# Kernel optimization log

Measured on AMD Instinct MI355X. Metric: run time of the kernel, lower is better.

Reference implementation:

```python
import jax, jax.numpy as jnp
import numpy as np


def setup_inputs() -> dict:
    key = jax.random.key(0)
    k1, k2, k3 = jax.random.split(key, 3)
    B, S, D_IN, V, D_OUT = 2, 2048, 1024, 32000, 4096
    x = jax.random.normal(k1, (B, S, D_IN), dtype=jnp.float32)
    W_ff = jax.random.normal(k2, (V, D_IN), dtype=jnp.float32) * (1.0 / np.sqrt(D_IN))
    b_ff = jnp.zeros((V,), dtype=jnp.float32)
    emb = jax.random.normal(k3, (V, D_OUT), dtype=jnp.float32)
    return {"x": x, "W_ff": W_ff, "b_ff": b_ff, "emb": emb}


def reference(x, W_ff, b_ff, emb):
    # logits: [B, S, V] = x @ W_ff^T + b
    logits = jnp.einsum('bsd,vd->bsv', x, W_ff) + b_ff
    probs = jax.nn.softmax(logits, axis=-1)  # [B, S, V]
    # soft embedding lookup: probs @ emb -> [B, S, D_OUT]
    out = jnp.einsum('bsv,vo->bso', probs, emb)
    return out
```

## Files before the change

### kernel.cpp

```cpp
#include <hip/hip_runtime.h>
#include <cstdint>

typedef unsigned short u16;
typedef __attribute__((ext_vector_type(8))) short short8;
typedef __attribute__((ext_vector_type(4))) short short4v;
typedef __attribute__((ext_vector_type(4))) float floatx4;

__device__ __forceinline__ u16 f2bf(float f) {
    unsigned u = __float_as_uint(f);
    return (u16)((u + 0x7FFFu + ((u >> 16) & 1u)) >> 16);
}
__device__ __forceinline__ float bf2f(u16 h) {
    return __uint_as_float(((unsigned)h) << 16);
}

__device__ __forceinline__ void gload16(u16* lds, const u16* g) {
    __builtin_amdgcn_global_load_lds(
        (const __attribute__((address_space(1))) unsigned*)g,
        (__attribute__((address_space(3))) unsigned*)lds,
        16, 0, 0);
}

#define CFENCE asm volatile("" ::: "memory")
#define MFMA16(a, b, c) __builtin_amdgcn_mfma_f32_16x16x32_bf16(a, b, c, 0, 0, 0)

__global__ void cast_kernel(const float* __restrict__ in, u16* __restrict__ out, int n4) {
    int stride = gridDim.x * blockDim.x;
    for (int i = blockIdx.x * blockDim.x + threadIdx.x; i < n4; i += stride) {
        float4 v = ((const float4*)in)[i];
        short4v o;
        o[0] = (short)f2bf(v.x);
        o[1] = (short)f2bf(v.y);
        o[2] = (short)f2bf(v.z);
        o[3] = (short)f2bf(v.w);
        ((short4v*)out)[i] = o;
    }
}

__global__ void transpose_cast(const float* __restrict__ E, u16* __restrict__ Et) {
    __shared__ u16 t[32][34];
    int bx = blockIdx.x, by = blockIdx.y;
    int x = threadIdx.x, y = threadIdx.y;
    long long c = (long long)bx * 32 + x;
    long long r0 = (long long)by * 32;
#pragma unroll
    for (int i = y; i < 32; i += 8)
        t[x][i] = f2bf(E[(r0 + i) * 4096 + c]);
    __syncthreads();
    int v = by * 32 + x;
#pragma unroll
    for (int i = y; i < 32; i += 8)
        Et[(long long)(bx * 32 + i) * 32000 + v] = t[i][x];
}

__global__ void rowsum_kernel(const u16* __restrict__ P, float* __restrict__ l, int V) {
    long long base = (long long)blockIdx.x * V;
    const short8* p8 = (const short8*)(P + base);
    int n8 = V >> 3;
    float s = 0.f;
    for (int c = threadIdx.x; c < n8; c += blockDim.x) {
        short8 v = p8[c];
#pragma unroll
        for (int j = 0; j < 8; ++j) s += bf2f((u16)v[j]);
    }
#pragma unroll
    for (int off = 32; off > 0; off >>= 1) s += __shfl_down(s, off, 64);
    __shared__ float red[4];
    if ((threadIdx.x & 63) == 0) red[threadIdx.x >> 6] = s;
    __syncthreads();
    if (threadIdx.x == 0) l[blockIdx.x] = red[0] + red[1] + red[2] + red[3];
}


template <int EP>
__global__ __launch_bounds__(512, 2)
void gemm8p(const u16* __restrict__ A, const u16* __restrict__ B,
            int M, int N, int K,
            const float* __restrict__ bias, u16* __restrict__ Pout,
            const float* __restrict__ rsum, float* __restrict__ Cout) {
    __shared__ u16 lds[2][2][2][128][64];
    const int tid = threadIdx.x;
    const int w = tid >> 6, lane = tid & 63;
    const int wm = w >> 2, wn = w & 3;
    const int fRow = lane & 15, fC = lane >> 4;
    const int wBase = w * 1024;

    int tm, tn;
    const int nTm = M >> 8;
    if (gridDim.x == 256) {
        const int x = blockIdx.x & 7, wgx = blockIdx.x >> 3;
        tm = (x & 3) * 4 + (wgx & 3);
        tn = (x >> 2) * 8 + (wgx >> 2);
    } else {
        const int q = gridDim.x >> 3;
        const int wg = (blockIdx.x & 7) * q + (blockIdx.x >> 3);
        tm = wg % nTm;
        tn = wg / nTm;
    }

    const u16* Abase = A + (long long)tm * 256 * K;
    const u16* Bbase = B + (long long)tn * 256 * K;
    const int NT = K >> 6;

    unsigned offA[4][2], offB[2][2];
#pragma unroll
    for (int m = 0; m < 4; ++m)
#pragma unroll
        for (int kk = 0; kk < 2; ++kk) {
            int R = wm * 64 + m * 16 + fRow;
            offA[m][kk] = (unsigned)(R * 64 + (((kk * 4 + fC) ^ ((R >> 1) & 7)) * 8));
        }
#pragma unroll
    for (int n = 0; n < 2; ++n)
#pragma unroll
        for (int kk = 0; kk < 2; ++kk) {
            int R = wn * 32 + n * 16 + fRow;
            offB[n][kk] = (unsigned)(R * 64 + (((kk * 4 + fC) ^ ((R >> 1) & 7)) * 8));
        }

    const u16 *pA0[2], *pA1[2], *pB0[2], *pB1[2];
#pragma unroll
    for (int i = 0; i < 2; ++i) {
        int r = w * 16 + i * 8 + (lane >> 3);
        int gcs = (lane & 7) ^ ((r >> 1) & 7);
        long long rowA = ((r >> 6) << 7) + (r & 63);
        long long rowB = ((r >> 5) << 6) + (r & 31);
        pA0[i] = Abase + rowA * K + gcs * 8;
        pA1[i] = Abase + (rowA + 64) * K + gcs * 8;
        pB0[i] = Bbase + rowB * K + gcs * 8;
        pB1[i] = Bbase + (rowB + 32) * K + gcs * 8;
    }

    floatx4 acc[8][4] = {};
    short8 af[4][2], bf0[2][2], bf1[2][2];

#pragma unroll
    for (int i = 0; i < 2; ++i) gload16(&lds[0][0][0][0][0] + wBase + i * 512, pA0[i]);
#pragma unroll
    for (int i = 0; i < 2; ++i) gload16(&lds[0][1][0][0][0] + wBase + i * 512, pB0[i]);
#pragma unroll
    for (int i = 0; i < 2; ++i) gload16(&lds[0][1][1][0][0] + wBase + i * 512, pB1[i]);
#pragma unroll
    for (int i = 0; i < 2; ++i) gload16(&lds[0][0][1][0][0] + wBase + i * 512, pA1[i]);
    if (NT > 1) {
#pragma unroll
        for (int i = 0; i < 2; ++i) gload16(&lds[1][0][0][0][0] + wBase + i * 512, pA0[i] + 64);
#pragma unroll
        for (int i = 0; i < 2; ++i) gload16(&lds[1][1][1][0][0] + wBase + i * 512, pB1[i] + 64);
#pragma unroll
        for (int i = 0; i < 2; ++i) gload16(&lds[1][0][1][0][0] + wBase + i * 512, pA1[i] + 64);
        asm volatile("s_waitcnt vmcnt(6)" ::: "memory");
    } else {
        asm volatile("s_waitcnt vmcnt(0)" ::: "memory");
    }
    __builtin_amdgcn_s_barrier();
    CFENCE;

#pragma unroll
    for (int i = 0; i < 2; ++i) {
        pB0[i] += 64;
        pA0[i] += 128;
        pB1[i] += 128;
        pA1[i] += 128;
    }

#pragma unroll
    for (int m = 0; m < 4; ++m)
#pragma unroll
        for (int kk = 0; kk < 2; ++kk)
            af[m][kk] = *(const short8*)(&lds[0][0][0][0][0] + offA[m][kk]);
#pragma unroll
    for (int n = 0; n < 2; ++n)
#pragma unroll
        for (int kk = 0; kk < 2; ++kk)
            bf1[n][kk] = *(const short8*)(&lds[0][1][1][0][0] + offB[n][kk]);

    for (int t = 0; t < NT; ++t) {
        const int d = t & 1;

#pragma unroll
        for (int n = 0; n < 2; ++n)
#pragma unroll
            for (int kk = 0; kk < 2; ++kk)
                bf0[n][kk] = *(const short8*)(&lds[d][1][0][0][0] + offB[n][kk]);
        if (t + 1 < NT) {
            gload16(&lds[d ^ 1][1][0][0][0] + wBase, pB0[0]);
            gload16(&lds[d ^ 1][1][0][0][0] + wBase + 512, pB0[1]);
        }
        asm volatile("s_waitcnt lgkmcnt(0)" ::: "memory");
        __builtin_amdgcn_sched_barrier(0);
        __builtin_amdgcn_s_setprio(1);
#pragma unroll
        for (int m = 0; m < 4; ++m)
#pragma unroll
            for (int n = 0; n < 2; ++n)
#pragma unroll
                for (int kk = 0; kk < 2; ++kk)
                    acc[m][n] = MFMA16(af[m][kk], bf0[n][kk], acc[m][n]);
        __builtin_amdgcn_s_setprio(0);
        __builtin_amdgcn_s_barrier();
        CFENCE;

        if (t + 2 < NT) {
            gload16(&lds[d][0][0][0][0] + wBase, pA0[0]);
            gload16(&lds[d][0][0][0][0] + wBase + 512, pA0[1]);
            gload16(&lds[d][1][1][0][0] + wBase, pB1[0]);
            gload16(&lds[d][1][1][0][0] + wBase + 512, pB1[1]);
        }
        __builtin_amdgcn_s_setprio(1);
#pragma unroll
        for (int m = 0; m < 4; ++m) {
#pragma unroll
            for (int n = 0; n < 2; ++n)
#pragma unroll
                for (int kk = 0; kk < 2; ++kk)
                    acc[m][2 + n] = MFMA16(af[m][kk], bf1[n][kk], acc[m][2 + n]);
#pragma unroll
            for (int kk = 0; kk < 2; ++kk)
                af[m][kk] = *(const short8*)(&lds[d][0][1][0][0] + offA[m][kk]);
        }
        __builtin_amdgcn_s_setprio(0);

        __builtin_amdgcn_s_setprio(1);
#pragma unroll
        for (int m = 0; m < 4; ++m)
#pragma unroll
            for (int n = 0; n < 2; ++n)
#pragma unroll
                for (int kk = 0; kk < 2; ++kk)
                    acc[4 + m][2 + n] = MFMA16(af[m][kk], bf1[n][kk], acc[4 + m][2 + n]);
        __builtin_amdgcn_s_setprio(0);

        if (t + 2 < NT) {
            asm volatile("s_waitcnt vmcnt(4)" ::: "memory");
        } else if (t + 1 < NT) {
            asm volatile("s_waitcnt vmcnt(0)" ::: "memory");
        }
        __builtin_amdgcn_s_barrier();
        CFENCE;
        if (t + 2 < NT) {
            gload16(&lds[d][0][1][0][0] + wBase, pA1[0]);
            gload16(&lds[d][0][1][0][0] + wBase + 512, pA1[1]);
        }
        if (t + 1 < NT) {
#pragma unroll
            for (int n = 0; n < 2; ++n)
#pragma unroll
                for (int kk = 0; kk < 2; ++kk)
                    bf1[n][kk] = *(const short8*)(&lds[d ^ 1][1][1][0][0] + offB[n][kk]);
            __builtin_amdgcn_s_setprio(1);
#pragma unroll
            for (int m = 0; m < 4; ++m) {
#pragma unroll
                for (int n = 0; n < 2; ++n)
#pragma unroll
                    for (int kk = 0; kk < 2; ++kk)
                        acc[4 + m][n] = MFMA16(af[m][kk], bf0[n][kk], acc[4 + m][n]);
#pragma unroll
                for (int kk = 0; kk < 2; ++kk)
                    af[m][kk] = *(const short8*)(&lds[d ^ 1][0][0][0][0] + offA[m][kk]);
            }
            __builtin_amdgcn_s_setprio(0);
        } else {
            __builtin_amdgcn_s_setprio(1);
#pragma unroll
            for (int m = 0; m < 4; ++m)
#pragma unroll
                for (int n = 0; n < 2; ++n)
#pragma unroll
                    for (int kk = 0; kk < 2; ++kk)
                        acc[4 + m][n] = MFMA16(af[m][kk], bf0[n][kk], acc[4 + m][n]);
            __builtin_amdgcn_s_setprio(0);
        }
#pragma unroll
        for (int i = 0; i < 2; ++i) {
            pB0[i] += 64;
            pA0[i] += 64;
            pB1[i] += 64;
            pA1[i] += 64;
        }
        CFENCE;
    }

    const int rBase = tm * 256 + wm * 128;
    const int cBase = tn * 256 + wn * 64;
    const int rOff = (lane >> 4) * 4;
    const int cOff = lane & 15;
#pragma unroll
    for (int m = 0; m < 8; ++m) {
#pragma unroll
        for (int n = 0; n < 4; ++n) {
            const int col = cBase + n * 16 + cOff;
            if (EP == 0) {
                float bv = bias[col];
#pragma unroll
                for (int r = 0; r < 4; ++r) {
                    int row = rBase + m * 16 + rOff + r;
                    Pout[(long long)row * N + col] = f2bf(__expf(acc[m][n][r] + bv));
                }
            } else {
#pragma unroll
                for (int r = 0; r < 4; ++r) {
                    int row = rBase + m * 16 + rOff + r;
                    Cout[(long long)row * N + col] = acc[m][n][r] * (1.0f / rsum[row]);
                }
            }
        }
    }
}

extern "C" void kernel_launch(void* const* d_in, const int* in_sizes, int n_in,
                              void* d_out, int out_size, void* d_ws, size_t ws_size,
                              hipStream_t stream) {
    const float* x = (const float*)d_in[0];
    const float* W = (const float*)d_in[1];
    const float* b = (const float*)d_in[2];
    const float* E = (const float*)d_in[3];
    float* out = (float*)d_out;

    const int M = 4096, K1 = 1024, V = 32000, N2 = 4096;

    char* ws = (char*)d_ws;
    size_t off = 0;
    u16* xb = (u16*)(ws + off); off += (size_t)M * K1 * 2;
    u16* Wb = (u16*)(ws + off); off += (size_t)V * K1 * 2;
    u16* Et = (u16*)(ws + off); off += (size_t)N2 * V * 2;
    u16* P  = (u16*)(ws + off); off += (size_t)M * V * 2;
    float* l = (float*)(ws + off); off += (size_t)M * 4;

    cast_kernel<<<2048, 256, 0, stream>>>(x, xb, M * K1 / 4);
    cast_kernel<<<2048, 256, 0, stream>>>(W, Wb, V * K1 / 4);
    transpose_cast<<<dim3(N2 / 32, V / 32), dim3(32, 8), 0, stream>>>(E, Et);
    gemm8p<0><<<(M / 256) * (V / 256), 512, 0, stream>>>(xb, Wb, M, V, K1, b, P, nullptr, nullptr);
    rowsum_kernel<<<M, 256, 0, stream>>>(P, l, V);
    gemm8p<1><<<(M / 256) * (N2 / 256), 512, 0, stream>>>(P, Et, M, N2, V, nullptr, nullptr, l, out);
}
```

Before: 1.391 ms.

## Fuse softmax row sums into first GEMM epilogue and vectorize transpose-cast

The exp epilogue of the logits GEMM now accumulates per-row partial sums in fp32, reduces them across lanes and waves through LDS, and writes one partial per column tile. A small kernel then sums those 125 partials per row, replacing the pass that reread the whole bf16 probability matrix. The embedding transpose-cast moves to 64x64 tiles with float4 loads and 16-byte stores. The sums now come from fp32 values instead of rounded bf16, and the GEMM epilogue gains extra registers, a block barrier and LDS use.

```diff
diff --git a/kernel.cpp b/kernel.cpp
--- a/kernel.cpp
+++ b/kernel.cpp
@@ -38,37 +38,39 @@
 }
 
 __global__ void transpose_cast(const float* __restrict__ E, u16* __restrict__ Et) {
-    __shared__ u16 t[32][34];
-    int bx = blockIdx.x, by = blockIdx.y;
-    int x = threadIdx.x, y = threadIdx.y;
-    long long c = (long long)bx * 32 + x;
-    long long r0 = (long long)by * 32;
-#pragma unroll
-    for (int i = y; i < 32; i += 8)
-        t[x][i] = f2bf(E[(r0 + i) * 4096 + c]);
+    __shared__ u16 t[64][68];
+    const int d0 = blockIdx.x * 64, v0 = blockIdx.y * 64;
+    const int tid = threadIdx.x;
+    const int lr = tid & 15, rr = tid >> 4;
+#pragma unroll
+    for (int it = 0; it < 4; ++it) {
+        int v = it * 16 + rr;
+        float4 e = *(const float4*)&E[(long long)(v0 + v) * 4096 + d0 + lr * 4];
+        t[lr * 4 + 0][v] = f2bf(e.x);
+        t[lr * 4 + 1][v] = f2bf(e.y);
+        t[lr * 4 + 2][v] = f2bf(e.z);
+        t[lr * 4 + 3][v] = f2bf(e.w);
+    }
     __syncthreads();
-    int v = by * 32 + x;
-#pragma unroll
-    for (int i = y; i < 32; i += 8)
-        Et[(long long)(bx * 32 + i) * 32000 + v] = t[i][x];
-}
-
-__global__ void rowsum_kernel(const u16* __restrict__ P, float* __restrict__ l, int V) {
-    long long base = (long long)blockIdx.x * V;
-    const short8* p8 = (const short8*)(P + base);
-    int n8 = V >> 3;
-    float s = 0.f;
-    for (int c = threadIdx.x; c < n8; c += blockDim.x) {
-        short8 v = p8[c];
-#pragma unroll
-        for (int j = 0; j < 8; ++j) s += bf2f((u16)v[j]);
-    }
-#pragma unroll
-    for (int off = 32; off > 0; off >>= 1) s += __shfl_down(s, off, 64);
-    __shared__ float red[4];
-    if ((threadIdx.x & 63) == 0) red[threadIdx.x >> 6] = s;
-    __syncthreads();
-    if (threadIdx.x == 0) l[blockIdx.x] = red[0] + red[1] + red[2] + red[3];
+    const int lc = tid & 7, rd = tid >> 3;
+#pragma unroll
+    for (int it = 0; it < 2; ++it) {
+        int dd = it * 32 + rd;
+        short8 o;
+#pragma unroll
+        for (int j = 0; j < 8; ++j) o[j] = (short)t[dd][lc * 8 + j];
+        *(short8*)&Et[(long long)(d0 + dd) * 32000 + v0 + lc * 8] = o;
+    }
+}
+
+__global__ void rowsum2(const float* __restrict__ Lp, float* __restrict__ l,
+                        int M, int ntn) {
+    int row = blockIdx.x * blockDim.x + threadIdx.x;
+    if (row < M) {
+        float s = 0.f;
+        for (int t = 0; t < ntn; ++t) s += Lp[(long long)t * M + row];
+        l[row] = s;
+    }
 }
 
 
@@ -77,8 +79,10 @@
 void gemm8p(const u16* __restrict__ A, const u16* __restrict__ B,
             int M, int N, int K,
             const float* __restrict__ bias, u16* __restrict__ Pout,
-            const float* __restrict__ rsum, float* __restrict__ Cout) {
+            const float* __restrict__ rsum, float* __restrict__ Cout,
+            float* __restrict__ Lp) {
     __shared__ u16 lds[2][2][2][128][64];
+    __shared__ float red[4][2][128];
     const int tid = threadIdx.x;
     const int w = tid >> 6, lane = tid & 63;
     const int wm = w >> 2, wn = w & 3;
@@ -286,6 +290,13 @@
     const int cBase = tn * 256 + wn * 64;
     const int rOff = (lane >> 4) * 4;
     const int cOff = lane & 15;
+    float rs[8][4];
+    if (EP == 0) {
+#pragma unroll
+        for (int m = 0; m < 8; ++m)
+#pragma unroll
+            for (int r = 0; r < 4; ++r) rs[m][r] = 0.f;
+    }
 #pragma unroll
     for (int m = 0; m < 8; ++m) {
 #pragma unroll
@@ -296,7 +307,9 @@
 #pragma unroll
                 for (int r = 0; r < 4; ++r) {
                     int row = rBase + m * 16 + rOff + r;
-                    Pout[(long long)row * N + col] = f2bf(__expf(acc[m][n][r] + bv));
+                    float e = __expf(acc[m][n][r] + bv);
+                    rs[m][r] += e;
+                    Pout[(long long)row * N + col] = f2bf(e);
                 }
             } else {
 #pragma unroll
@@ -305,6 +318,24 @@
                     Cout[(long long)row * N + col] = acc[m][n][r] * (1.0f / rsum[row]);
                 }
             }
+        }
+    }
+    if (EP == 0) {
+#pragma unroll
+        for (int m = 0; m < 8; ++m)
+#pragma unroll
+            for (int r = 0; r < 4; ++r) {
+                float s = rs[m][r];
+#pragma unroll
+                for (int mk = 1; mk < 16; mk <<= 1) s += __shfl_xor(s, mk, 64);
+                if ((lane & 15) == 0) red[wn][wm][m * 16 + rOff + r] = s;
+            }
+        __syncthreads();
+        if (tid < 256) {
+            int wmm = tid >> 7, rr = tid & 127;
+            float s = red[0][wmm][rr] + red[1][wmm][rr] +
+                      red[2][wmm][rr] + red[3][wmm][rr];
+            Lp[(long long)tn * M + tm * 256 + wmm * 128 + rr] = s;
         }
     }
 }
@@ -319,6 +350,7 @@
     float* out = (float*)d_out;
 
     const int M = 4096, K1 = 1024, V = 32000, N2 = 4096;
+    const int NTN1 = V / 256;
 
     char* ws = (char*)d_ws;
     size_t off = 0;
@@ -326,12 +358,13 @@
     u16* Wb = (u16*)(ws + off); off += (size_t)V * K1 * 2;
     u16* Et = (u16*)(ws + off); off += (size_t)N2 * V * 2;
     u16* P  = (u16*)(ws + off); off += (size_t)M * V * 2;
-    float* l = (float*)(ws + off); off += (size_t)M * 4;
+    float* l  = (float*)(ws + off); off += (size_t)M * 4;
+    float* Lp = (float*)(ws + off); off += (size_t)NTN1 * M * 4;
 
     cast_kernel<<<2048, 256, 0, stream>>>(x, xb, M * K1 / 4);
     cast_kernel<<<2048, 256, 0, stream>>>(W, Wb, V * K1 / 4);
-    transpose_cast<<<dim3(N2 / 32, V / 32), dim3(32, 8), 0, stream>>>(E, Et);
-    gemm8p<0><<<(M / 256) * (V / 256), 512, 0, stream>>>(xb, Wb, M, V, K1, b, P, nullptr, nullptr);
-    rowsum_kernel<<<M, 256, 0, stream>>>(P, l, V);
-    gemm8p<1><<<(M / 256) * (N2 / 256), 512, 0, stream>>>(P, Et, M, N2, V, nullptr, nullptr, l, out);
-}
+    transpose_cast<<<dim3(N2 / 64, V / 64), 256, 0, stream>>>(E, Et);
+    gemm8p<0><<<(M / 256) * (V / 256), 512, 0, stream>>>(xb, Wb, M, V, K1, b, P, nullptr, nullptr, Lp);
+    rowsum2<<<M / 256, 256, 0, stream>>>(Lp, l, M, NTN1);
+    gemm8p<1><<<(M / 256) * (N2 / 256), 512, 0, stream>>>(P, Et, M, N2, V, nullptr, nullptr, l, out, nullptr);
+}
```

Result: slower. 1.423 ms (+2.3%).
